# Kernel optimization log

Hardware: AMD Instinct MI355X
Metric: run time of the kernel (lower is better)

Reference implementation:

```python
import jax, jax.numpy as jnp
import numpy as np


def setup_inputs() -> dict:
    key = jax.random.key(0)
    k1, k2 = jax.random.split(key)
    B, C, H, W, K = 8, 32, 224, 224, 5
    x = jax.random.normal(k1, (B, C, H, W), dtype=jnp.float32)
    kernel = jax.random.normal(k2, (C, 1, K, K), dtype=jnp.float32) * 0.1
    return {"x": x, "kernel": kernel, "stride": 1, "padding": 2, "dilation": 1}


def reference(x, kernel, stride, padding, dilation):
    # Tropical-max (morphological dilation) conv: out[p] = max_k (x[p+k] + w_flipped[k]).
    # is_max=True, softmax_temp=None -> hard max; kernel is flipped (true convolution).
    B, C, H, W = x.shape
    OC, _, K, _ = kernel.shape
    neutral = -jnp.inf
    x_pad = jnp.pad(x, ((0, 0), (0, 0), (padding, padding), (padding, padding)),
                    constant_values=neutral)
    Hp, Wp = H + 2 * padding, W + 2 * padding
    H_out = (Hp - dilation * (K - 1) - 1) // stride + 1
    W_out = (Wp - dilation * (K - 1) - 1) // stride + 1
    wflip = kernel[:, 0, ::-1, ::-1]  # (C, K, K) flipped, as in torch kernel.flip((2,3))
    # Start from neutral: matches the extra neutral row padded onto the unfold tensor.
    out = jnp.full((B, C, H_out, W_out), neutral, dtype=x.dtype)
    for i in range(K):  # small fixed K*K loop; avoids materializing the (B,C,K^2,HW) unfold
        for j in range(K):
            patch = x_pad[:, :,
                          i * dilation: i * dilation + (H_out - 1) * stride + 1: stride,
                          j * dilation: j * dilation + (W_out - 1) * stride + 1: stride]
            out = jnp.maximum(out, patch + wflip[:, i, j][None, :, None, None])
    return out
```

## Files before the change

### kernel.cpp

```cpp
#include <hip/hip_runtime.h>
#include <math.h>


#define TC_B 8
#define TC_C 32
#define TC_H 224
#define TC_W 224
#define TC_WQ (TC_W / 4)

__global__ __launch_bounds__(256) void tropical_conv2d_kernel(
    const float* __restrict__ x, const float* __restrict__ kern,
    float* __restrict__ out) {
  const int wq = threadIdx.x;
  const int hl = threadIdx.y;
  const int blk = blockIdx.x;
  const int hgroup = blk % (TC_H / 4);
  const int bc = blk / (TC_H / 4);
  const int c = bc % TC_C;
  const int h = hgroup * 4 + hl;

  __shared__ float wk[25];
  const int t = hl * 64 + wq;
  if (t < 25) wk[t] = kern[c * 25 + 24 - t];
  __syncthreads();

  if (wq >= TC_WQ) return;

  const float* xp = x + (size_t)bc * (TC_H * TC_W);
  const float NEG = -INFINITY;

  float acc0 = NEG, acc1 = NEG, acc2 = NEG, acc3 = NEG;

  #pragma unroll
  for (int i = 0; i < 5; ++i) {
    const int r = h - 2 + i;
    if (r < 0 || r >= TC_H) continue;
    const float4* row = (const float4*)(xp + (size_t)r * TC_W);
    float4 a, b, cc;
    if (wq > 0)        a  = row[wq - 1];
    else               a  = make_float4(NEG, NEG, NEG, NEG);
    b = row[wq];
    if (wq < TC_WQ - 1) cc = row[wq + 1];
    else                cc = make_float4(NEG, NEG, NEG, NEG);

    float v[12] = {a.x, a.y, a.z, a.w, b.x, b.y, b.z, b.w, cc.x, cc.y, cc.z, cc.w};

    #pragma unroll
    for (int j = 0; j < 5; ++j) {
      const float w = wk[i * 5 + j];
      acc0 = fmaxf(acc0, v[2 + j] + w);
      acc1 = fmaxf(acc1, v[3 + j] + w);
      acc2 = fmaxf(acc2, v[4 + j] + w);
      acc3 = fmaxf(acc3, v[5 + j] + w);
    }
  }

  float4 res = make_float4(acc0, acc1, acc2, acc3);
  ((float4*)(out + (size_t)bc * (TC_H * TC_W) + (size_t)h * TC_W))[wq] = res;
}

extern "C" void kernel_launch(void* const* d_in, const int* in_sizes, int n_in,
                              void* d_out, int out_size, void* d_ws, size_t ws_size,
                              hipStream_t stream) {
  const float* x = (const float*)d_in[0];
  const float* k = (const float*)d_in[1];
  float* out = (float*)d_out;

  dim3 block(64, 4, 1);
  dim3 grid(TC_B * TC_C * (TC_H / 4), 1, 1);
  tropical_conv2d_kernel<<<grid, block, 0, stream>>>(x, k, out);
}
```

Baseline: 124.1 us.

## Compute four output rows per thread to reuse loaded input rows

Result: faster. 121.4 us (-2.2%).

```diff
diff --git a/kernel.cpp b/kernel.cpp
--- a/kernel.cpp
+++ b/kernel.cpp
@@ -7,6 +7,7 @@
 #define TC_H 224
 #define TC_W 224
 #define TC_WQ (TC_W / 4)
+#define TC_HG (TC_H / 16)
 
 __global__ __launch_bounds__(256) void tropical_conv2d_kernel(
     const float* __restrict__ x, const float* __restrict__ kern,
@@ -14,10 +15,9 @@
   const int wq = threadIdx.x;
   const int hl = threadIdx.y;
   const int blk = blockIdx.x;
-  const int hgroup = blk % (TC_H / 4);
-  const int bc = blk / (TC_H / 4);
+  const int hg = blk % TC_HG;
+  const int bc = blk / TC_HG;
   const int c = bc % TC_C;
-  const int h = hgroup * 4 + hl;
 
   __shared__ float wk[25];
   const int t = hl * 64 + wq;
@@ -26,37 +26,64 @@
 
   if (wq >= TC_WQ) return;
 
+  const int hbase = hg * 16 + hl * 4;
   const float* xp = x + (size_t)bc * (TC_H * TC_W);
   const float NEG = -INFINITY;
 
-  float acc0 = NEG, acc1 = NEG, acc2 = NEG, acc3 = NEG;
+  float acc[4][4];
+  #pragma unroll
+  for (int o = 0; o < 4; ++o)
+    #pragma unroll
+    for (int k = 0; k < 4; ++k) acc[o][k] = NEG;
 
   #pragma unroll
-  for (int i = 0; i < 5; ++i) {
-    const int r = h - 2 + i;
-    if (r < 0 || r >= TC_H) continue;
-    const float4* row = (const float4*)(xp + (size_t)r * TC_W);
-    float4 a, b, cc;
-    if (wq > 0)        a  = row[wq - 1];
-    else               a  = make_float4(NEG, NEG, NEG, NEG);
-    b = row[wq];
-    if (wq < TC_WQ - 1) cc = row[wq + 1];
-    else                cc = make_float4(NEG, NEG, NEG, NEG);
-
-    float v[12] = {a.x, a.y, a.z, a.w, b.x, b.y, b.z, b.w, cc.x, cc.y, cc.z, cc.w};
+  for (int ri = 0; ri < 8; ++ri) {
+    const int r = hbase + ri - 2;
+    float v[12];
+    if (r >= 0 && r < TC_H) {
+      const float4* row = (const float4*)(xp + (size_t)r * TC_W);
+      float4 b = row[wq];
+      float4 a, cc;
+      if (wq > 0)          a  = row[wq - 1];
+      else                 a  = make_float4(NEG, NEG, NEG, NEG);
+      if (wq < TC_WQ - 1)  cc = row[wq + 1];
+      else                 cc = make_float4(NEG, NEG, NEG, NEG);
+      v[0]=a.x; v[1]=a.y; v[2]=a.z; v[3]=a.w;
+      v[4]=b.x; v[5]=b.y; v[6]=b.z; v[7]=b.w;
+      v[8]=cc.x; v[9]=cc.y; v[10]=cc.z; v[11]=cc.w;
+    } else {
+      #pragma unroll
+      for (int q = 0; q < 12; ++q) v[q] = NEG;
+    }
 
     #pragma unroll
-    for (int j = 0; j < 5; ++j) {
-      const float w = wk[i * 5 + j];
-      acc0 = fmaxf(acc0, v[2 + j] + w);
-      acc1 = fmaxf(acc1, v[3 + j] + w);
-      acc2 = fmaxf(acc2, v[4 + j] + w);
-      acc3 = fmaxf(acc3, v[5 + j] + w);
+    for (int o = 0; o < 4; ++o) {
+      const int i = ri - o;
+      if (i < 0 || i > 4) continue;
+      const float w0 = wk[i * 5 + 0];
+      const float w1 = wk[i * 5 + 1];
+      const float w2 = wk[i * 5 + 2];
+      const float w3 = wk[i * 5 + 3];
+      const float w4 = wk[i * 5 + 4];
+      #pragma unroll
+      for (int k = 0; k < 4; ++k) {
+        const float t0 = v[2 + k] + w0;
+        const float t1 = v[3 + k] + w1;
+        const float t2 = v[4 + k] + w2;
+        const float t3 = v[5 + k] + w3;
+        const float t4 = v[6 + k] + w4;
+        const float m = fmaxf(fmaxf(t0, t1), fmaxf(fmaxf(t2, t3), t4));
+        acc[o][k] = fmaxf(acc[o][k], m);
+      }
     }
   }
 
-  float4 res = make_float4(acc0, acc1, acc2, acc3);
-  ((float4*)(out + (size_t)bc * (TC_H * TC_W) + (size_t)h * TC_W))[wq] = res;
+  float* op = out + (size_t)bc * (TC_H * TC_W);
+  #pragma unroll
+  for (int o = 0; o < 4; ++o) {
+    ((float4*)(op + (size_t)(hbase + o) * TC_W))[wq] =
+        make_float4(acc[o][0], acc[o][1], acc[o][2], acc[o][3]);
+  }
 }
 
 extern "C" void kernel_launch(void* const* d_in, const int* in_sizes, int n_in,
@@ -67,6 +94,6 @@
   float* out = (float*)d_out;
 
   dim3 block(64, 4, 1);
-  dim3 grid(TC_B * TC_C * (TC_H / 4), 1, 1);
+  dim3 grid(TC_B * TC_C * TC_HG, 1, 1);
   tropical_conv2d_kernel<<<grid, block, 0, stream>>>(x, k, out);
 }
```
